# Optimization experiments

Hardware: AMD Instinct MI355X
Metric: run time of the kernel (lower is better)

## Reference

```python
import jax, jax.numpy as jnp
import numpy as np

D_MODEL = 1024
N_HEADS = 16
D_K = D_MODEL // N_HEADS


def setup_inputs() -> dict:
    key = jax.random.key(0)
    ks = jax.random.split(key, 7)
    s = 1.0 / np.sqrt(D_MODEL)
    return {
        "x": jax.random.normal(ks[0], (2, 2048, D_MODEL), dtype=jnp.float32),
        "w_q": jax.random.uniform(ks[1], (D_MODEL, D_MODEL), jnp.float32, -s, s),
        "w_k": jax.random.uniform(ks[2], (D_MODEL, D_MODEL), jnp.float32, -s, s),
        "w_v": jax.random.uniform(ks[3], (D_MODEL, D_MODEL), jnp.float32, -s, s),
        "w_o": jax.random.uniform(ks[4], (D_MODEL, D_MODEL), jnp.float32, -s, s),
        "b_o": jax.random.uniform(ks[5], (D_MODEL,), jnp.float32, -s, s),
        "ln_gamma": jnp.ones((D_MODEL,), jnp.float32),
        "ln_beta": jnp.zeros((D_MODEL,), jnp.float32),
    }


def reference(x, w_q, w_k, w_v, w_o, b_o, ln_gamma, ln_beta):
    # Pre-LN
    mu = jnp.mean(x, axis=-1, keepdims=True)
    var = jnp.mean(jnp.square(x - mu), axis=-1, keepdims=True)
    x_norm = (x - mu) / jnp.sqrt(var + 1e-5) * ln_gamma + ln_beta

    B, S, _ = x.shape
    # torch Linear: y = x @ W.T ; weights stored [out, in]
    def proj(w):
        return (x_norm @ w.T).reshape(B, S, N_HEADS, D_K).transpose(0, 2, 1, 3)

    Q, K, V = proj(w_q), proj(w_k), proj(w_v)  # [B,H,S,Dk]
    scores = jnp.einsum("bhqd,bhkd->bhqk", Q, K) / np.sqrt(D_K)
    attn = jax.nn.softmax(scores, axis=-1)
    attended = jnp.einsum("bhqk,bhkd->bhqd", attn, V)
    attended = attended.transpose(0, 2, 1, 3).reshape(B, S, D_MODEL)
    out = attended @ w_o.T + b_o
    return x + out
```

## Files before the change

### kernel.cpp

```cpp
#include <hip/hip_runtime.h>

typedef _Float16 f16;
typedef _Float16 f16x8 __attribute__((ext_vector_type(8)));
typedef _Float16 f16x4 __attribute__((ext_vector_type(4)));
typedef _Float16 f16x2 __attribute__((ext_vector_type(2)));
typedef __fp16 fp16x2 __attribute__((ext_vector_type(2)));
typedef float f32x4 __attribute__((ext_vector_type(4)));

#define SEQ   2048
#define DM    1024
#define DKH   64
#define MTOT  4096

__device__ __forceinline__ f32x4 mfma16(f16x8 a, f16x8 b, f32x4 c) {
  return __builtin_amdgcn_mfma_f32_16x16x32_f16(a, b, c, 0, 0, 0);
}

__device__ __forceinline__ f16x2 cvt_pk(float a, float b) {
  fp16x2 r = __builtin_amdgcn_cvt_pkrtz(a, b);
  return __builtin_bit_cast(f16x2, r);
}

__device__ __forceinline__ void gload16(const f16* g, f16* l) {
  __builtin_amdgcn_global_load_lds(
      (const __attribute__((address_space(1))) void*)g,
      (__attribute__((address_space(3))) void*)l, 16, 0, 0);
}

__global__ __launch_bounds__(256) void prep_kernel(const float* __restrict__ x,
                                                   const float* __restrict__ w_q,
                                                   const float* __restrict__ w_k,
                                                   const float* __restrict__ w_v,
                                                   const float* __restrict__ w_o,
                                                   const float* __restrict__ gamma,
                                                   const float* __restrict__ beta,
                                                   f16* __restrict__ wout,
                                                   f16* __restrict__ xn) {
  const int t = threadIdx.x;
  if (blockIdx.x < 4096) {
    const int sel = blockIdx.x >> 10;
    const float* src = sel == 0 ? w_q : sel == 1 ? w_k : sel == 2 ? w_v : w_o;
    const int i = ((blockIdx.x & 1023) * 256 + t) * 4;
    float4 v = *reinterpret_cast<const float4*>(src + i);
    f16x4 o;
    o[0] = (f16)v.x; o[1] = (f16)v.y; o[2] = (f16)v.z; o[3] = (f16)v.w;
    *reinterpret_cast<f16x4*>(wout + (size_t)sel * 1048576 + i) = o;
    return;
  }
  const int row = blockIdx.x - 4096;
  const float* xr = x + (size_t)row * DM;
  float v[4], s = 0.f, s2 = 0.f;
#pragma unroll
  for (int i = 0; i < 4; ++i) {
    v[i] = xr[t + i * 256];
    s += v[i];
    s2 += v[i] * v[i];
  }
#pragma unroll
  for (int o = 32; o > 0; o >>= 1) {
    s  += __shfl_down(s, o);
    s2 += __shfl_down(s2, o);
  }
  __shared__ float ps[4], ps2[4], mu_s, rs_s;
  if ((t & 63) == 0) { ps[t >> 6] = s; ps2[t >> 6] = s2; }
  __syncthreads();
  if (t == 0) {
    float a = ps[0] + ps[1] + ps[2] + ps[3];
    float b = ps2[0] + ps2[1] + ps2[2] + ps2[3];
    float mu = a * (1.f / DM);
    float var = b * (1.f / DM) - mu * mu;
    mu_s = mu;
    rs_s = rsqrtf(var + 1e-5f);
  }
  __syncthreads();
  const float mu = mu_s, rs = rs_s;
#pragma unroll
  for (int i = 0; i < 4; ++i) {
    int d = t + i * 256;
    xn[(size_t)row * DM + d] = (f16)(((v[i] - mu) * rs) * gamma[d] + beta[d]);
  }
}

__global__ __launch_bounds__(256) void gemm_qkv(const f16* __restrict__ A,
                                                const f16* __restrict__ Wqkv,
                                                f16* __restrict__ qb,
                                                f16* __restrict__ kb,
                                                f16* __restrict__ vtb) {
  __shared__ f16 sA[128][64];
  __shared__ f16 sB[64][64];
  const int t = threadIdx.x, l = t & 63, w = t >> 6;
  const int wr = w >> 1, wc = w & 1, lg = l >> 4, lm = l & 15;
  const int m0 = blockIdx.y * 128, n0 = blockIdx.x * 64;
  const int crow = l >> 3;
  const int scol = ((l & 7) ^ crow) << 3;
  const int rsw  = (lm & 7) << 3;

  f32x4 acc[4][2] = {};

  for (int k0 = 0; k0 < DM; k0 += 64) {
    __syncthreads();
#pragma unroll
    for (int cc = 0; cc < 4; ++cc) {
      const int c = w + cc * 4;
      gload16(A + (size_t)(m0 + c * 8 + crow) * DM + k0 + scol, &sA[c * 8][0]);
    }
#pragma unroll
    for (int cc = 0; cc < 2; ++cc) {
      const int c = w + cc * 4;
      gload16(Wqkv + (size_t)(n0 + c * 8 + crow) * DM + k0 + scol, &sB[c * 8][0]);
    }
    __syncthreads();
#pragma unroll
    for (int kk = 0; kk < 2; ++kk) {
      f16x8 af[4], bf[2];
#pragma unroll
      for (int i = 0; i < 4; ++i)
        af[i] = *(const f16x8*)&sA[wr * 64 + i * 16 + lm][(kk * 32 + lg * 8) ^ rsw];
#pragma unroll
      for (int i = 0; i < 2; ++i)
        bf[i] = *(const f16x8*)&sB[wc * 32 + i * 16 + lm][(kk * 32 + lg * 8) ^ rsw];
#pragma unroll
      for (int mi = 0; mi < 4; ++mi)
#pragma unroll
        for (int ni = 0; ni < 2; ++ni)
          acc[mi][ni] = mfma16(af[mi], bf[ni], acc[mi][ni]);
    }
  }

  const int sel = blockIdx.x >> 4;
  if (sel < 2) {
    f16* outp = sel == 0 ? qb : kb;
    const int nloc = n0 - sel * 1024;
#pragma unroll
    for (int mi = 0; mi < 4; ++mi) {
      const int rowb = m0 + wr * 64 + mi * 16 + lg * 4;
#pragma unroll
      for (int ni = 0; ni < 2; ++ni) {
        const int col = nloc + wc * 32 + ni * 16 + lm;
#pragma unroll
        for (int r = 0; r < 4; ++r)
          outp[(size_t)(rowb + r) * DM + col] = (f16)acc[mi][ni][r];
      }
    }
  } else {
#pragma unroll
    for (int mi = 0; mi < 4; ++mi) {
      const int rowb = m0 + wr * 64 + mi * 16 + lg * 4;
      const int b = rowb >> 11, s = rowb & 2047;
#pragma unroll
      for (int ni = 0; ni < 2; ++ni) {
        const int col = (n0 - 2048) + wc * 32 + ni * 16 + lm;
        f16x4 o;
        o[0] = (f16)acc[mi][ni][0]; o[1] = (f16)acc[mi][ni][1];
        o[2] = (f16)acc[mi][ni][2]; o[3] = (f16)acc[mi][ni][3];
        *reinterpret_cast<f16x4*>(&vtb[(size_t)(b * 1024 + col) * SEQ + s]) = o;
      }
    }
  }
}

__global__ __launch_bounds__(256) void gemm_out(const f16* __restrict__ A,
                                                const f16* __restrict__ W,
                                                float* __restrict__ out,
                                                const float* __restrict__ bias,
                                                const float* __restrict__ resid) {
  __shared__ f16 sA[128][64];
  __shared__ f16 sB[64][64];
  const int t = threadIdx.x, l = t & 63, w = t >> 6;
  const int wr = w >> 1, wc = w & 1, lg = l >> 4, lm = l & 15;
  const int m0 = blockIdx.y * 128, n0 = blockIdx.x * 64;
  const int crow = l >> 3;
  const int scol = ((l & 7) ^ crow) << 3;
  const int rsw  = (lm & 7) << 3;

  f32x4 acc[4][2] = {};

  for (int k0 = 0; k0 < DM; k0 += 64) {
    __syncthreads();
#pragma unroll
    for (int cc = 0; cc < 4; ++cc) {
      const int c = w + cc * 4;
      gload16(A + (size_t)(m0 + c * 8 + crow) * DM + k0 + scol, &sA[c * 8][0]);
    }
#pragma unroll
    for (int cc = 0; cc < 2; ++cc) {
      const int c = w + cc * 4;
      gload16(W + (size_t)(n0 + c * 8 + crow) * DM + k0 + scol, &sB[c * 8][0]);
    }
    __syncthreads();
#pragma unroll
    for (int kk = 0; kk < 2; ++kk) {
      f16x8 af[4], bf[2];
#pragma unroll
      for (int i = 0; i < 4; ++i)
        af[i] = *(const f16x8*)&sA[wr * 64 + i * 16 + lm][(kk * 32 + lg * 8) ^ rsw];
#pragma unroll
      for (int i = 0; i < 2; ++i)
        bf[i] = *(const f16x8*)&sB[wc * 32 + i * 16 + lm][(kk * 32 + lg * 8) ^ rsw];
#pragma unroll
      for (int mi = 0; mi < 4; ++mi)
#pragma unroll
        for (int ni = 0; ni < 2; ++ni)
          acc[mi][ni] = mfma16(af[mi], bf[ni], acc[mi][ni]);
    }
  }

#pragma unroll
  for (int mi = 0; mi < 4; ++mi) {
    const int rowb = m0 + wr * 64 + mi * 16 + lg * 4;
#pragma unroll
    for (int ni = 0; ni < 2; ++ni) {
      const int col = n0 + wc * 32 + ni * 16 + lm;
#pragma unroll
      for (int r = 0; r < 4; ++r) {
        const size_t idx = (size_t)(rowb + r) * DM + col;
        out[idx] = resid[idx] + bias[col] + acc[mi][ni][r];
      }
    }
  }
}

__global__ __launch_bounds__(512, 4) void attn_kernel(const f16* __restrict__ Qb,
                                                      const f16* __restrict__ Kb,
                                                      const f16* __restrict__ Vt,
                                                      f16* __restrict__ Ob) {
  __shared__ __align__(16) char smem[65536];
  f16 (*sK)[2][64][64] = (f16(*)[2][64][64])smem;
  f16 (*sV)[2][64][64] = (f16(*)[2][64][64])(smem + 32768);
  float* cb = (float*)smem;

  int bx = blockIdx.x;
  bx = (bx & 7) * 64 + (bx >> 3);
  const int qt = bx & 15, bh = bx >> 4;
  const int h = bh & 15, b = bh >> 4;
  const int t = threadIdx.x, l = t & 63, w = t >> 6;
  const int kg = w >> 2, wq = w & 3;
  const int lg = l >> 4, lm = l & 15;
  const float K2 = 0.18033688f;

  f16x8 qf[2][2];
#pragma unroll
  for (int qg = 0; qg < 2; ++qg) {
    const f16* qptr =
        Qb + (size_t)(b * SEQ + qt * 128 + wq * 32 + qg * 16 + lm) * DM + h * DKH;
    qf[qg][0] = *(const f16x8*)(qptr + lg * 8);
    qf[qg][1] = *(const f16x8*)(qptr + 32 + lg * 8);
#pragma unroll
    for (int j = 0; j < 8; ++j) {
      qf[qg][0][j] = (f16)((float)qf[qg][0][j] * K2);
      qf[qg][1][j] = (f16)((float)qf[qg][1][j] * K2);
    }
  }

  const f16x8 ones = {(f16)1, (f16)1, (f16)1, (f16)1,
                      (f16)1, (f16)1, (f16)1, (f16)1};

  f32x4 oacc[2][4] = {};
  f32x4 oden[2] = {};

  const int crow = l >> 3;
  const int scol = ((l & 7) ^ crow) << 3;
  const int rsw  = (lm & 7) << 3;

  const f16* kptr[2];
  const f16* vptr[2];
#pragma unroll
  for (int cc = 0; cc < 2; ++cc) {
    const int c = wq + cc * 4;
    const int krow = c * 8 + crow;
    const int nfp = krow >> 4, lgp = (krow >> 2) & 3, rp = krow & 3;
    const int key = (nfp >> 1) * 32 + lgp * 8 + (nfp & 1) * 4 + rp;
    kptr[cc] = Kb + (size_t)(b * SEQ + kg * 1024 + key) * DM + h * DKH + scol;
    vptr[cc] = Vt + (size_t)(bh * DKH + c * 8 + crow) * SEQ + kg * 1024 + scol;
  }

  auto stage = [&](int buf) {
#pragma unroll
    for (int cc = 0; cc < 2; ++cc) {
      const int c = wq + cc * 4;
      gload16(kptr[cc], &sK[kg][buf][c * 8][0]);
      gload16(vptr[cc], &sV[kg][buf][c * 8][0]);
      kptr[cc] += 64 * DM;
      vptr[cc] += 64;
    }
  };

  stage(0);
  __syncthreads();
  int cur = 0;

  union PU { f16x8 v; f16x2 hh[4]; };

  for (int kt = 0; kt < 16; ++kt) {
    if (kt < 15) stage(cur ^ 1);

    f32x4 sc[2][4] = {};
    __builtin_amdgcn_s_setprio(1);
#pragma unroll
    for (int kk = 0; kk < 2; ++kk)
#pragma unroll
      for (int nf = 0; nf < 4; ++nf) {
        f16x8 kf = *(const f16x8*)
            &sK[kg][cur][nf * 16 + lm][(kk * 32 + lg * 8) ^ rsw];
        sc[0][nf] = mfma16(kf, qf[0][kk], sc[0][nf]);
        sc[1][nf] = mfma16(kf, qf[1][kk], sc[1][nf]);
      }
    __builtin_amdgcn_s_setprio(0);

    PU pu[2][2];
#pragma unroll
    for (int qg = 0; qg < 2; ++qg)
#pragma unroll
      for (int nf = 0; nf < 4; ++nf) {
        float e0 = __builtin_amdgcn_exp2f(sc[qg][nf][0]);
        float e1 = __builtin_amdgcn_exp2f(sc[qg][nf][1]);
        float e2 = __builtin_amdgcn_exp2f(sc[qg][nf][2]);
        float e3 = __builtin_amdgcn_exp2f(sc[qg][nf][3]);
        pu[qg][nf >> 1].hh[(nf & 1) * 2 + 0] = cvt_pk(e0, e1);
        pu[qg][nf >> 1].hh[(nf & 1) * 2 + 1] = cvt_pk(e2, e3);
      }

    __builtin_amdgcn_s_setprio(1);
#pragma unroll
    for (int ks = 0; ks < 2; ++ks) {
#pragma unroll
      for (int ni = 0; ni < 4; ++ni) {
        f16x8 vf = *(const f16x8*)
            &sV[kg][cur][ni * 16 + lm][(ks * 32 + lg * 8) ^ rsw];
        oacc[0][ni] = mfma16(pu[0][ks].v, vf, oacc[0][ni]);
        oacc[1][ni] = mfma16(pu[1][ks].v, vf, oacc[1][ni]);
      }
      oden[0] = mfma16(pu[0][ks].v, ones, oden[0]);
      oden[1] = mfma16(pu[1][ks].v, ones, oden[1]);
    }
    __builtin_amdgcn_s_setprio(0);

    __syncthreads();
    cur ^= 1;
  }

  float* myp = cb + (size_t)(wq * 64 + l) * 40;
  if (kg == 1) {
#pragma unroll
    for (int qg = 0; qg < 2; ++qg)
#pragma unroll
      for (int ni = 0; ni < 4; ++ni)
#pragma unroll
        for (int r = 0; r < 4; ++r) myp[qg * 16 + ni * 4 + r] = oacc[qg][ni][r];
#pragma unroll
    for (int qg = 0; qg < 2; ++qg)
#pragma unroll
      for (int r = 0; r < 4; ++r) myp[32 + qg * 4 + r] = oden[qg][r];
  }
  __syncthreads();
  if (kg == 0) {
#pragma unroll
    for (int qg = 0; qg < 2; ++qg) {
#pragma unroll
      for (int ni = 0; ni < 4; ++ni)
#pragma unroll
        for (int r = 0; r < 4; ++r) oacc[qg][ni][r] += myp[qg * 16 + ni * 4 + r];
      float rd[4];
#pragma unroll
      for (int r = 0; r < 4; ++r)
        rd[r] = 1.f / (oden[qg][r] + myp[32 + qg * 4 + r]);
#pragma unroll
      for (int ni = 0; ni < 4; ++ni)
#pragma unroll
        for (int r = 0; r < 4; ++r) {
          const int q = qt * 128 + wq * 32 + qg * 16 + lg * 4 + r;
          const int d = ni * 16 + lm;
          Ob[(size_t)(b * SEQ + q) * DM + h * DKH + d] =
              (f16)(oacc[qg][ni][r] * rd[r]);
        }
    }
  }
}

extern "C" void kernel_launch(void* const* d_in, const int* in_sizes, int n_in,
                              void* d_out, int out_size, void* d_ws, size_t ws_size,
                              hipStream_t stream) {
  const float* x   = (const float*)d_in[0];
  const float* w_q = (const float*)d_in[1];
  const float* w_k = (const float*)d_in[2];
  const float* w_v = (const float*)d_in[3];
  const float* w_o = (const float*)d_in[4];
  const float* b_o = (const float*)d_in[5];
  const float* lng = (const float*)d_in[6];
  const float* lnb = (const float*)d_in[7];
  float* out = (float*)d_out;

  char* ws = (char*)d_ws;
  const size_t MB = 1ull << 20;
  f16* xn   = (f16*)(ws + 0 * MB);
  f16* wqkv = (f16*)(ws + 8 * MB);
  f16* woh  = (f16*)(ws + 14 * MB);
  f16* qb   = (f16*)(ws + 16 * MB);
  f16* kb   = (f16*)(ws + 24 * MB);
  f16* vtb  = (f16*)(ws + 32 * MB);
  f16* att  = (f16*)(ws + 40 * MB);

  prep_kernel<<<8192, 256, 0, stream>>>(x, w_q, w_k, w_v, w_o, lng, lnb, wqkv, xn);
  gemm_qkv<<<dim3(48, 32), 256, 0, stream>>>(xn, wqkv, qb, kb, vtb);
  attn_kernel<<<512, 512, 0, stream>>>(qb, kb, vtb, att);
  gemm_out<<<dim3(16, 32), 256, 0, stream>>>(att, woh, out, b_o, x);
}
```

Measured before the change: 108.5 us.

## Double-buffer LDS tiles in QKV and output GEMMs with prefetch

Both projection GEMMs now keep two LDS buffers per operand. The next K-tile's global-to-LDS load is issued before the current tile's MFMAs, and there is one barrier per iteration instead of two. MFMA sections are also wrapped in s_setprio so waves in the compute phase get issue priority. This aims to overlap global load latency with matrix math, at the cost of doubled LDS use, which may lower occupancy. Correctness depends on the async LDS loads being complete at the barrier.

```diff
diff --git a/kernel.cpp b/kernel.cpp
--- a/kernel.cpp
+++ b/kernel.cpp
@@ -86,8 +86,8 @@
                                                 f16* __restrict__ qb,
                                                 f16* __restrict__ kb,
                                                 f16* __restrict__ vtb) {
-  __shared__ f16 sA[128][64];
-  __shared__ f16 sB[64][64];
+  __shared__ f16 sA[2][128][64];
+  __shared__ f16 sB[2][64][64];
   const int t = threadIdx.x, l = t & 63, w = t >> 6;
   const int wr = w >> 1, wc = w & 1, lg = l >> 4, lm = l & 15;
   const int m0 = blockIdx.y * 128, n0 = blockIdx.x * 64;
@@ -97,34 +97,44 @@
 
   f32x4 acc[4][2] = {};
 
-  for (int k0 = 0; k0 < DM; k0 += 64) {
-    __syncthreads();
+  auto stage = [&](int buf, int k0) {
 #pragma unroll
     for (int cc = 0; cc < 4; ++cc) {
       const int c = w + cc * 4;
-      gload16(A + (size_t)(m0 + c * 8 + crow) * DM + k0 + scol, &sA[c * 8][0]);
+      gload16(A + (size_t)(m0 + c * 8 + crow) * DM + k0 + scol, &sA[buf][c * 8][0]);
     }
 #pragma unroll
     for (int cc = 0; cc < 2; ++cc) {
       const int c = w + cc * 4;
-      gload16(Wqkv + (size_t)(n0 + c * 8 + crow) * DM + k0 + scol, &sB[c * 8][0]);
-    }
-    __syncthreads();
+      gload16(Wqkv + (size_t)(n0 + c * 8 + crow) * DM + k0 + scol, &sB[buf][c * 8][0]);
+    }
+  };
+
+  stage(0, 0);
+  __syncthreads();
+  int cur = 0;
+
+  for (int it = 0; it < DM / 64; ++it) {
+    if (it < DM / 64 - 1) stage(cur ^ 1, (it + 1) * 64);
 #pragma unroll
     for (int kk = 0; kk < 2; ++kk) {
       f16x8 af[4], bf[2];
 #pragma unroll
       for (int i = 0; i < 4; ++i)
-        af[i] = *(const f16x8*)&sA[wr * 64 + i * 16 + lm][(kk * 32 + lg * 8) ^ rsw];
+        af[i] = *(const f16x8*)&sA[cur][wr * 64 + i * 16 + lm][(kk * 32 + lg * 8) ^ rsw];
 #pragma unroll
       for (int i = 0; i < 2; ++i)
-        bf[i] = *(const f16x8*)&sB[wc * 32 + i * 16 + lm][(kk * 32 + lg * 8) ^ rsw];
+        bf[i] = *(const f16x8*)&sB[cur][wc * 32 + i * 16 + lm][(kk * 32 + lg * 8) ^ rsw];
+      __builtin_amdgcn_s_setprio(1);
 #pragma unroll
       for (int mi = 0; mi < 4; ++mi)
 #pragma unroll
         for (int ni = 0; ni < 2; ++ni)
           acc[mi][ni] = mfma16(af[mi], bf[ni], acc[mi][ni]);
-    }
+      __builtin_amdgcn_s_setprio(0);
+    }
+    __syncthreads();
+    cur ^= 1;
   }
 
   const int sel = blockIdx.x >> 4;
@@ -164,8 +174,8 @@
                                                 float* __restrict__ out,
                                                 const float* __restrict__ bias,
                                                 const float* __restrict__ resid) {
-  __shared__ f16 sA[128][64];
-  __shared__ f16 sB[64][64];
+  __shared__ f16 sA[2][128][64];
+  __shared__ f16 sB[2][64][64];
   const int t = threadIdx.x, l = t & 63, w = t >> 6;
   const int wr = w >> 1, wc = w & 1, lg = l >> 4, lm = l & 15;
   const int m0 = blockIdx.y * 128, n0 = blockIdx.x * 64;
@@ -175,34 +185,44 @@
 
   f32x4 acc[4][2] = {};
 
-  for (int k0 = 0; k0 < DM; k0 += 64) {
-    __syncthreads();
+  auto stage = [&](int buf, int k0) {
 #pragma unroll
     for (int cc = 0; cc < 4; ++cc) {
       const int c = w + cc * 4;
-      gload16(A + (size_t)(m0 + c * 8 + crow) * DM + k0 + scol, &sA[c * 8][0]);
+      gload16(A + (size_t)(m0 + c * 8 + crow) * DM + k0 + scol, &sA[buf][c * 8][0]);
     }
 #pragma unroll
     for (int cc = 0; cc < 2; ++cc) {
       const int c = w + cc * 4;
-      gload16(W + (size_t)(n0 + c * 8 + crow) * DM + k0 + scol, &sB[c * 8][0]);
-    }
-    __syncthreads();
+      gload16(W + (size_t)(n0 + c * 8 + crow) * DM + k0 + scol, &sB[buf][c * 8][0]);
+    }
+  };
+
+  stage(0, 0);
+  __syncthreads();
+  int cur = 0;
+
+  for (int it = 0; it < DM / 64; ++it) {
+    if (it < DM / 64 - 1) stage(cur ^ 1, (it + 1) * 64);
 #pragma unroll
     for (int kk = 0; kk < 2; ++kk) {
       f16x8 af[4], bf[2];
 #pragma unroll
       for (int i = 0; i < 4; ++i)
-        af[i] = *(const f16x8*)&sA[wr * 64 + i * 16 + lm][(kk * 32 + lg * 8) ^ rsw];
+        af[i] = *(const f16x8*)&sA[cur][wr * 64 + i * 16 + lm][(kk * 32 + lg * 8) ^ rsw];
 #pragma unroll
       for (int i = 0; i < 2; ++i)
-        bf[i] = *(const f16x8*)&sB[wc * 32 + i * 16 + lm][(kk * 32 + lg * 8) ^ rsw];
+        bf[i] = *(const f16x8*)&sB[cur][wc * 32 + i * 16 + lm][(kk * 32 + lg * 8) ^ rsw];
+      __builtin_amdgcn_s_setprio(1);
 #pragma unroll
       for (int mi = 0; mi < 4; ++mi)
 #pragma unroll
         for (int ni = 0; ni < 2; ++ni)
           acc[mi][ni] = mfma16(af[mi], bf[ni], acc[mi][ni]);
-    }
+      __builtin_amdgcn_s_setprio(0);
+    }
+    __syncthreads();
+    cur ^= 1;
   }
 
 #pragma unroll
```

Measured after the change: 105.4 us. -2.9%, faster.
